# Performance work log

Measured on AMD Instinct MI355X. Metric: run time of the kernel, lower is better.

The kernel has to match this reference:

```python
import jax, jax.numpy as jnp
import numpy as np

B = 4
MAX_N = 2048
D = 512
H = 8
HD = D // H
SRC_LENS = [2048, 1536, 1800, 1200]   # sum = 6584
REF_LENS = [1900, 2048, 1400, 1600]   # sum = 6948
NEG_INF = -1e9


def setup_inputs() -> dict:
    key = jax.random.key(0)
    ks = jax.random.split(key, 8)
    n_src, n_ref = sum(SRC_LENS), sum(REF_LENS)
    s = 0.02
    return {
        "feats_src": jax.random.normal(ks[0], (n_src, D), dtype=jnp.float32),
        "batch_src": jnp.asarray(np.repeat(np.arange(B), SRC_LENS), dtype=jnp.int32),
        "feats_ref": jax.random.normal(ks[1], (n_ref, D), dtype=jnp.float32),
        "batch_ref": jnp.asarray(np.repeat(np.arange(B), REF_LENS), dtype=jnp.int32),
        "w_in": jax.random.normal(ks[2], (3 * D, D), dtype=jnp.float32) * s,
        "b_in": jnp.zeros((3 * D,), dtype=jnp.float32),
        "w_out": jax.random.normal(ks[3], (D, D), dtype=jnp.float32) * s,
        "b_out": jnp.zeros((D,), dtype=jnp.float32),
        "gw1": jax.random.normal(ks[4], (D, D), dtype=jnp.float32) * s,
        "gb1": jnp.zeros((D,), dtype=jnp.float32),
        "gw2": jax.random.normal(ks[5], (1, D), dtype=jnp.float32) * s,
        "gb2": jnp.zeros((1,), dtype=jnp.float32),
    }


def _to_dense(feats, batch_idx):
    # sparse [N, D] (sorted batch indices) -> dense [B, MAX_N, D] + key_padding_mask
    n = feats.shape[0]
    counts = jax.ops.segment_sum(jnp.ones((n,), jnp.int32), batch_idx, num_segments=B)
    starts = jnp.concatenate([jnp.zeros((1,), jnp.int32), jnp.cumsum(counts)[:-1].astype(jnp.int32)])
    pos = jnp.arange(n, dtype=jnp.int32) - starts[batch_idx]  # position within batch
    dense = jnp.zeros((B, MAX_N, feats.shape[1]), feats.dtype).at[batch_idx, pos].set(feats)
    mask = jnp.arange(MAX_N)[None, :] >= counts[:, None]  # True = padding (key_padding_mask)
    return dense, mask, pos


def reference(feats_src, batch_src, feats_ref, batch_ref,
              w_in, b_in, w_out, b_out, gw1, gb1, gw2, gb2):
    d_src, mask_src, pos_src = _to_dense(feats_src, batch_src)
    d_ref, mask_ref, _ = _to_dense(feats_ref, batch_ref)

    # nn.MultiheadAttention (batch_first, eval mode): packed in_proj, scaled dot-product
    q = (d_src @ w_in[:D].T + b_in[:D]).reshape(B, MAX_N, H, HD)
    k = (d_ref @ w_in[D:2 * D].T + b_in[D:2 * D]).reshape(B, MAX_N, H, HD)
    v = (d_ref @ w_in[2 * D:].T + b_in[2 * D:]).reshape(B, MAX_N, H, HD)
    scores = jnp.einsum('bqhd,bkhd->bhqk', q * (HD ** -0.5), k)
    scores = jnp.where(mask_ref[:, None, None, :], NEG_INF, scores)
    attn = jax.nn.softmax(scores, axis=-1)
    ctx = jnp.einsum('bhqk,bkhd->bqhd', attn, v).reshape(B, MAX_N, D)
    d_aligned = ctx @ w_out.T + b_out

    # gate MLP: Linear -> ReLU -> Linear -> Sigmoid
    gate = jax.nn.sigmoid(jax.nn.relu(d_aligned @ gw1.T + gb1) @ gw2.T + gb2)  # [B, MAX_N, 1]
    d_out = d_src + gate * d_aligned

    # dense -> ragged: gather each token back to its flat slot
    out_flat = d_out[batch_src, pos_src]  # [N_src, D]
    return out_flat, gate
```

## Files before the change

### kernel.cpp

```cpp
#include <hip/hip_runtime.h>
#include <hip/hip_bf16.h>


typedef __bf16 bf16x8_t __attribute__((ext_vector_type(8)));
typedef __bf16 bf16x4_t __attribute__((ext_vector_type(4)));
typedef float f32x4_t __attribute__((ext_vector_type(4)));
typedef float f32x2_t __attribute__((ext_vector_type(2)));

#define CQ_SCALE 0.18033688011112042f

__device__ inline bf16x8_t zero8() {
  bf16x8_t z;
#pragma unroll
  for (int t = 0; t < 8; ++t) z[t] = (__bf16)0.0f;
  return z;
}

__device__ __forceinline__ int sniff_f32(const void* w) {
  unsigned short u = ((const unsigned short*)w)[threadIdx.x & 63];
  return __ballot((u & 0x7F80) >= 0x3F80) != 0ULL;
}

__global__ void sentinel_k(float* out) {
  if (threadIdx.x == 0 && blockIdx.x == 0) out[0] = 1000.0f;
}

__global__ void cv_all(const void* w_in, const void* b_in, const void* w_out,
                       const void* b_out, const void* gw1, const void* gb1,
                       const void* gw2, const void* gb2,
                       __hip_bfloat16* __restrict__ ws) {
  int f = sniff_f32(w_in);
  const size_t F_W_IN = 16, F_B_IN = 786448, F_W_OUT = 787984, F_B_OUT = 1050128,
               F_GW1 = 1050640, F_GB1 = 1312784, F_GW2 = 1313296, F_GB2 = 1313808;
  const int total = 1313793;
  for (int g = blockIdx.x * 256 + threadIdx.x; g < total; g += gridDim.x * 256) {
    const void* src;
    size_t dst;
    int i;
    if (g < 786432) { src = w_in; dst = F_W_IN; i = g; }
    else if (g < 787968) { src = b_in; dst = F_B_IN; i = g - 786432; }
    else if (g < 1050112) { src = w_out; dst = F_W_OUT; i = g - 787968; }
    else if (g < 1050624) { src = b_out; dst = F_B_OUT; i = g - 1050112; }
    else if (g < 1312768) { src = gw1; dst = F_GW1; i = g - 1050624; }
    else if (g < 1313280) { src = gb1; dst = F_GB1; i = g - 1312768; }
    else if (g < 1313792) { src = gw2; dst = F_GW2; i = g - 1313280; }
    else { src = gb2; dst = F_GB2; i = g - 1313792; }
    ws[dst + i] = f ? __float2bfloat16(((const float*)src)[i])
                    : ((const __hip_bfloat16*)src)[i];
  }
}

__device__ __forceinline__ void gemm_core(
    const void* __restrict__ A_, long aoff, const __hip_bfloat16* __restrict__ Bt,
    const __hip_bfloat16* __restrict__ bias, __hip_bfloat16* __restrict__ C,
    int M, int K, int lda, int ldc, float cscale, int relu, int f, int bm, int bn,
    long chs, __bf16 (&As)[128][64], __bf16 (&Bs)[128][64]) {
  int tid = threadIdx.x, lane = tid & 63, wave = tid >> 6;
  int wm = wave >> 1, wn = wave & 1;
  int l15 = lane & 15, quad = lane >> 4;

  f32x4_t acc[4][4];
#pragma unroll
  for (int i = 0; i < 4; ++i)
#pragma unroll
    for (int j = 0; j < 4; ++j)
#pragma unroll
      for (int r = 0; r < 4; ++r) acc[i][j][r] = 0.f;

  bf16x8_t ra[4], rb[4];
  f32x4_t raf[4][2];

  auto gload = [&](int k0) {
#pragma unroll
    for (int s = 0; s < 4; ++s) {
      int id = s * 256 + tid;
      int row = id >> 3, col = (id & 7) * 8;
      int arow = bm + row;
      if (f) {
        if (arow < M) {
          const float* p = (const float*)A_ + aoff + (size_t)arow * lda + k0 + col;
          raf[s][0] = *reinterpret_cast<const f32x4_t*>(p);
          raf[s][1] = *reinterpret_cast<const f32x4_t*>(p + 4);
        } else {
#pragma unroll
          for (int e = 0; e < 4; ++e) { raf[s][0][e] = 0.f; raf[s][1][e] = 0.f; }
        }
      } else {
        ra[s] = (arow < M)
                    ? *reinterpret_cast<const bf16x8_t*>((const __hip_bfloat16*)A_ + aoff +
                                                         (size_t)arow * lda + k0 + col)
                    : zero8();
      }
      rb[s] = *reinterpret_cast<const bf16x8_t*>(Bt + (size_t)(bn + row) * 512 + k0 + col);
    }
  };
  auto stage = [&]() {
#pragma unroll
    for (int s = 0; s < 4; ++s) {
      int id = s * 256 + tid;
      int row = id >> 3, col = (id & 7) * 8;
      if (f) {
        bf16x8_t t;
#pragma unroll
        for (int e = 0; e < 4; ++e) {
          t[e] = (__bf16)raf[s][0][e];
          t[4 + e] = (__bf16)raf[s][1][e];
        }
        *reinterpret_cast<bf16x8_t*>(&As[row][col]) = t;
      } else {
        *reinterpret_cast<bf16x8_t*>(&As[row][col]) = ra[s];
      }
      *reinterpret_cast<bf16x8_t*>(&Bs[row][col]) = rb[s];
    }
  };

  int nk = K >> 6;
  gload(0);
  for (int it = 0; it < nk; ++it) {
    stage();
    __syncthreads();
    if (it + 1 < nk) gload((it + 1) * 64);
#pragma unroll
    for (int ks = 0; ks < 2; ++ks) {
      bf16x8_t af[4], bfv[4];
#pragma unroll
      for (int i = 0; i < 4; ++i)
        af[i] = *reinterpret_cast<const bf16x8_t*>(
            &As[wm * 64 + i * 16 + l15][ks * 32 + quad * 8]);
#pragma unroll
      for (int j = 0; j < 4; ++j)
        bfv[j] = *reinterpret_cast<const bf16x8_t*>(
            &Bs[wn * 64 + j * 16 + l15][ks * 32 + quad * 8]);
#pragma unroll
      for (int i = 0; i < 4; ++i)
#pragma unroll
        for (int j = 0; j < 4; ++j)
          acc[i][j] = __builtin_amdgcn_mfma_f32_16x16x32_bf16(af[i], bfv[j], acc[i][j], 0, 0, 0);
    }
    __syncthreads();
  }

#pragma unroll
  for (int i = 0; i < 4; ++i)
#pragma unroll
    for (int j = 0; j < 4; ++j) {
      int col = bn + wn * 64 + j * 16 + l15;
      float bv = __bfloat162float(bias[col]);
#pragma unroll
      for (int r = 0; r < 4; ++r) {
        int row = bm + wm * 64 + i * 16 + quad * 4 + r;
        if (row < M) {
          float v = (acc[i][j][r] + bv) * cscale;
          if (relu) v = fmaxf(v, 0.f);
          size_t idx = chs ? ((size_t)(col >> 6) * chs + (size_t)row * 64 + (col & 63))
                           : ((size_t)row * ldc + col);
          C[idx] = __float2bfloat16(v);
        }
      }
    }
}

__global__ __launch_bounds__(256) void proj2(
    const void* __restrict__ fs, const void* __restrict__ fr,
    const __hip_bfloat16* __restrict__ ws, __hip_bfloat16* __restrict__ Q,
    __hip_bfloat16* __restrict__ KV, const void* snf) {
  __shared__ __bf16 As[128][64];
  __shared__ __bf16 Bs[128][64];
  const size_t F_W_IN = 16, F_B_IN = 786448;
  const long CHS = (long)6948 * 64;
  int f = sniff_f32(snf);
  int bid = blockIdx.x;
  if (bid < 208) {
    int bx = bid >> 2, by = bid & 3;
    gemm_core(fs, 0, ws + F_W_IN, ws + F_B_IN, Q, 6584, 512, 512, 512, CQ_SCALE, 0, f,
              bx * 128, by * 128, 0, As, Bs);
  } else {
    int k = bid - 208;
    int bx = k >> 3, by = k & 7;
    gemm_core(fr, 0, ws + F_W_IN + 262144, ws + F_B_IN + 512, KV, 6948, 512, 512, 1024,
              1.0f, 0, f, bx * 128, by * 128, CHS, As, Bs);
  }
}

template <bool AF32>
__global__ __launch_bounds__(256) void gemm128(
    const void* __restrict__ A_, long aoff, const __hip_bfloat16* __restrict__ Bt,
    const __hip_bfloat16* __restrict__ bias, __hip_bfloat16* __restrict__ C,
    int M, int K, int lda, int ldc, float cscale, int relu, long chs,
    const void* snf) {
  __shared__ __bf16 As[128][64];
  __shared__ __bf16 Bs[128][64];
  int f = 0;
  if constexpr (AF32) f = sniff_f32(snf);
  gemm_core(A_, aoff, Bt, bias, C, M, K, lda, ldc, cscale, relu, f,
            blockIdx.x * 128, blockIdx.y * 128, chs, As, Bs);
}

template <int NS>
__global__ __launch_bounds__(256) void gemm128_pv(
    const __hip_bfloat16* __restrict__ P, const float* __restrict__ L,
    const __hip_bfloat16* __restrict__ Bt, const __hip_bfloat16* __restrict__ bias,
    __hip_bfloat16* __restrict__ C, int M) {
  const size_t PSZ = 3375104;
  __shared__ __bf16 As[128][64];
  __shared__ __bf16 Bs[128][64];
  int tid = threadIdx.x, lane = tid & 63, wave = tid >> 6;
  int wm = wave >> 1, wn = wave & 1;
  int l15 = lane & 15, quad = lane >> 4;
  int bm = blockIdx.x * 128, bn = blockIdx.y * 128;

  f32x4_t acc[4][4];
#pragma unroll
  for (int i = 0; i < 4; ++i)
#pragma unroll
    for (int j = 0; j < 4; ++j)
#pragma unroll
      for (int r = 0; r < 4; ++r) acc[i][j][r] = 0.f;

  bf16x8_t rp[NS][4], rb[4];
  float rl[4][NS];

  auto gload = [&](int k0) {
    int h = k0 >> 6;
#pragma unroll
    for (int s = 0; s < 4; ++s) {
      int id = s * 256 + tid;
      int row = id >> 3, col = (id & 7) * 8;
      int arow = bm + row;
      if (arow < M) {
        size_t off = (size_t)arow * 512 + k0 + col;
#pragma unroll
        for (int i = 0; i < NS; ++i)
          rp[i][s] = *reinterpret_cast<const bf16x8_t*>(P + i * PSZ + off);
        const float* lp = &L[((size_t)arow * 8 + h) * NS];
#pragma unroll
        for (int i = 0; i < NS; ++i) rl[s][i] = lp[i];
      } else {
#pragma unroll
        for (int i = 0; i < NS; ++i) rp[i][s] = zero8();
        rl[s][0] = 1.f;
#pragma unroll
        for (int i = 1; i < NS; ++i) rl[s][i] = 0.f;
      }
      rb[s] = *reinterpret_cast<const bf16x8_t*>(Bt + (size_t)(bn + row) * 512 + k0 + col);
    }
  };
  auto stage = [&]() {
#pragma unroll
    for (int s = 0; s < 4; ++s) {
      int id = s * 256 + tid;
      int row = id >> 3, col = (id & 7) * 8;
      float sum = 0.f;
#pragma unroll
      for (int i = 0; i < NS; ++i) sum += rl[s][i];
      float sc = 1.0f / sum;
      bf16x8_t t;
#pragma unroll
      for (int e = 0; e < 8; ++e) {
        float v = 0.f;
#pragma unroll
        for (int i = 0; i < NS; ++i) v += rl[s][i] * (float)rp[i][s][e];
        t[e] = (__bf16)(v * sc);
      }
      *reinterpret_cast<bf16x8_t*>(&As[row][col]) = t;
      *reinterpret_cast<bf16x8_t*>(&Bs[row][col]) = rb[s];
    }
  };

  gload(0);
  for (int it = 0; it < 8; ++it) {
    stage();
    __syncthreads();
    if (it + 1 < 8) gload((it + 1) * 64);
#pragma unroll
    for (int ks = 0; ks < 2; ++ks) {
      bf16x8_t af[4], bfv[4];
#pragma unroll
      for (int i = 0; i < 4; ++i)
        af[i] = *reinterpret_cast<const bf16x8_t*>(
            &As[wm * 64 + i * 16 + l15][ks * 32 + quad * 8]);
#pragma unroll
      for (int j = 0; j < 4; ++j)
        bfv[j] = *reinterpret_cast<const bf16x8_t*>(
            &Bs[wn * 64 + j * 16 + l15][ks * 32 + quad * 8]);
#pragma unroll
      for (int i = 0; i < 4; ++i)
#pragma unroll
        for (int j = 0; j < 4; ++j)
          acc[i][j] = __builtin_amdgcn_mfma_f32_16x16x32_bf16(af[i], bfv[j], acc[i][j], 0, 0, 0);
    }
    __syncthreads();
  }

#pragma unroll
  for (int i = 0; i < 4; ++i)
#pragma unroll
    for (int j = 0; j < 4; ++j) {
      int col = bn + wn * 64 + j * 16 + l15;
      float bv = __bfloat162float(bias[col]);
#pragma unroll
      for (int r = 0; r < 4; ++r) {
        int row = bm + wm * 64 + i * 16 + quad * 4 + r;
        if (row < M)
          C[(size_t)row * 512 + col] = __float2bfloat16(acc[i][j][r] + bv);
      }
    }
}

__device__ __forceinline__ void flash_core(
    const __hip_bfloat16* __restrict__ Qb, const __hip_bfloat16* __restrict__ Kb,
    const __hip_bfloat16* __restrict__ Vb, __hip_bfloat16* __restrict__ OUTb,
    float* __restrict__ LPb, int lns, int nsrc, int nref, int qt, int kt0,
    int ktNfull, int do_tail, __bf16 (&VtL)[2][64][72], __bf16 (&PL)[4][32][72]) {
  int h = blockIdx.y;
  int tid = threadIdx.x, lane = tid & 63, wave = tid >> 6;
  int l15 = lane & 15, quad = lane >> 4;
  int Mb = nsrc + 1;
  int qbase = qt * 128 + wave * 32;

  bf16x8_t qfr[2][2];
#pragma unroll
  for (int g = 0; g < 2; ++g) {
    int qrow = qbase + g * 16 + l15;
#pragma unroll
    for (int ks = 0; ks < 2; ++ks)
      qfr[g][ks] = (qrow < nsrc)
                       ? *reinterpret_cast<const bf16x8_t*>(
                             Qb + (size_t)qrow * 512 + h * 64 + ks * 32 + quad * 8)
                       : zero8();
  }

  f32x4_t O[2][4];
#pragma unroll
  for (int g = 0; g < 2; ++g)
#pragma unroll
    for (int j = 0; j < 4; ++j)
#pragma unroll
      for (int r = 0; r < 4; ++r) O[g][j][r] = 0.f;

  f32x4_t Lacc[2];
#pragma unroll
  for (int g = 0; g < 2; ++g)
#pragma unroll
    for (int r = 0; r < 4; ++r) Lacc[g][r] = 0.f;
  bf16x8_t ones;
#pragma unroll
  for (int t = 0; t < 8; ++t) ones[t] = (__bf16)1.0f;

  bf16x8_t kf[8], v0, v1;
  auto loadK = [&](int k0) {
#pragma unroll
    for (int j = 0; j < 4; ++j) {
      const __hip_bfloat16* kp = Kb + (size_t)(k0 + j * 16 + l15) * 64 + quad * 8;
      kf[j * 2] = *reinterpret_cast<const bf16x8_t*>(kp);
      kf[j * 2 + 1] = *reinterpret_cast<const bf16x8_t*>(kp + 32);
    }
  };
  auto loadV = [&](int k0) {
    const __hip_bfloat16* vp = Vb + (size_t)(k0 + lane) * 64 + wave * 16;
    v0 = *reinterpret_cast<const bf16x8_t*>(vp);
    v1 = *reinterpret_cast<const bf16x8_t*>(vp + 8);
  };

  int nit = ktNfull - kt0;
  if (nit > 0) {
    loadK(kt0 * 64);
    loadV(kt0 * 64);
  }

  for (int it = 0; it < nit; ++it) {
    int k0 = (kt0 + it) * 64;
    __bf16(*Vt)[72] = VtL[it & 1];
#pragma unroll
    for (int e = 0; e < 8; ++e) {
      Vt[wave * 16 + e][lane] = v0[e];
      Vt[wave * 16 + 8 + e][lane] = v1[e];
    }
    if (it + 1 < nit) loadV(k0 + 64);

#pragma unroll
    for (int g = 0; g < 2; ++g) {
      f32x4_t St[4];
#pragma unroll
      for (int j = 0; j < 4; ++j)
#pragma unroll
        for (int r = 0; r < 4; ++r) St[j][r] = 0.f;
#pragma unroll
      for (int j = 0; j < 4; ++j)
#pragma unroll
        for (int ks = 0; ks < 2; ++ks)
          St[j] = __builtin_amdgcn_mfma_f32_16x16x32_bf16(kf[j * 2 + ks], qfr[g][ks],
                                                          St[j], 0, 0, 0);
#pragma unroll
      for (int j = 0; j < 4; ++j) {
        bf16x4_t pk;
#pragma unroll
        for (int r = 0; r < 4; ++r) pk[r] = (__bf16)exp2f(St[j][r]);
        *reinterpret_cast<bf16x4_t*>(&PL[wave][g * 16 + l15][j * 16 + quad * 4]) = pk;
      }
    }
    if (it + 1 < nit) loadK(k0 + 64);

    __syncthreads();

    bf16x8_t pa[2][2];
#pragma unroll
    for (int g = 0; g < 2; ++g)
#pragma unroll
      for (int ks = 0; ks < 2; ++ks)
        pa[g][ks] = *reinterpret_cast<const bf16x8_t*>(
            &PL[wave][g * 16 + l15][ks * 32 + quad * 8]);
#pragma unroll
    for (int g = 0; g < 2; ++g)
#pragma unroll
      for (int ks = 0; ks < 2; ++ks)
        Lacc[g] = __builtin_amdgcn_mfma_f32_16x16x32_bf16(pa[g][ks], ones, Lacc[g], 0, 0, 0);
#pragma unroll
    for (int j = 0; j < 4; ++j)
#pragma unroll
      for (int ks = 0; ks < 2; ++ks) {
        bf16x8_t vbf =
            *reinterpret_cast<const bf16x8_t*>(&Vt[j * 16 + l15][ks * 32 + quad * 8]);
#pragma unroll
        for (int g = 0; g < 2; ++g)
          O[g][j] = __builtin_amdgcn_mfma_f32_16x16x32_bf16(pa[g][ks], vbf, O[g][j], 0, 0, 0);
      }
  }

  if (do_tail) {
    int k0 = ktNfull * 64;
    __bf16(*Vt)[72] = VtL[nit & 1];
    {
      int kr = k0 + lane;
      const __hip_bfloat16* vp = Vb + (size_t)kr * 64 + wave * 16;
      bf16x8_t t0 = (kr < nref) ? *reinterpret_cast<const bf16x8_t*>(vp) : zero8();
      bf16x8_t t1 = (kr < nref) ? *reinterpret_cast<const bf16x8_t*>(vp + 8) : zero8();
#pragma unroll
      for (int e = 0; e < 8; ++e) {
        Vt[wave * 16 + e][lane] = t0[e];
        Vt[wave * 16 + 8 + e][lane] = t1[e];
      }
    }
#pragma unroll
    for (int j = 0; j < 4; ++j) {
      int kcol = k0 + j * 16 + l15;
      const __hip_bfloat16* kp = Kb + (size_t)kcol * 64 + quad * 8;
      kf[j * 2] = (kcol < nref) ? *reinterpret_cast<const bf16x8_t*>(kp) : zero8();
      kf[j * 2 + 1] = (kcol < nref) ? *reinterpret_cast<const bf16x8_t*>(kp + 32) : zero8();
    }
#pragma unroll
    for (int g = 0; g < 2; ++g) {
      f32x4_t St[4];
#pragma unroll
      for (int j = 0; j < 4; ++j)
#pragma unroll
        for (int r = 0; r < 4; ++r) St[j][r] = 0.f;
#pragma unroll
      for (int j = 0; j < 4; ++j)
#pragma unroll
        for (int ks = 0; ks < 2; ++ks)
          St[j] = __builtin_amdgcn_mfma_f32_16x16x32_bf16(kf[j * 2 + ks], qfr[g][ks],
                                                          St[j], 0, 0, 0);
#pragma unroll
      for (int j = 0; j < 4; ++j) {
        bf16x4_t pk;
#pragma unroll
        for (int r = 0; r < 4; ++r) {
          int kl = k0 + j * 16 + quad * 4 + r;
          pk[r] = (__bf16)((kl < nref) ? exp2f(St[j][r]) : 0.f);
        }
        *reinterpret_cast<bf16x4_t*>(&PL[wave][g * 16 + l15][j * 16 + quad * 4]) = pk;
      }
    }
    __syncthreads();
    bf16x8_t pa[2][2];
#pragma unroll
    for (int g = 0; g < 2; ++g)
#pragma unroll
      for (int ks = 0; ks < 2; ++ks)
        pa[g][ks] = *reinterpret_cast<const bf16x8_t*>(
            &PL[wave][g * 16 + l15][ks * 32 + quad * 8]);
#pragma unroll
    for (int g = 0; g < 2; ++g)
#pragma unroll
      for (int ks = 0; ks < 2; ++ks)
        Lacc[g] = __builtin_amdgcn_mfma_f32_16x16x32_bf16(pa[g][ks], ones, Lacc[g], 0, 0, 0);
#pragma unroll
    for (int j = 0; j < 4; ++j)
#pragma unroll
      for (int ks = 0; ks < 2; ++ks) {
        bf16x8_t vbf =
            *reinterpret_cast<const bf16x8_t*>(&Vt[j * 16 + l15][ks * 32 + quad * 8]);
#pragma unroll
        for (int g = 0; g < 2; ++g)
          O[g][j] = __builtin_amdgcn_mfma_f32_16x16x32_bf16(pa[g][ks], vbf, O[g][j], 0, 0, 0);
      }
  }

  if (LPb && l15 == 0) {
#pragma unroll
    for (int g = 0; g < 2; ++g)
#pragma unroll
      for (int r = 0; r < 4; ++r) {
        int row = qbase + g * 16 + quad * 4 + r;
        if (row < Mb) LPb[((size_t)row * 8 + h) * lns] = Lacc[g][r];
      }
  }

#pragma unroll
  for (int g = 0; g < 2; ++g)
#pragma unroll
    for (int r = 0; r < 4; ++r) {
      int row = qbase + g * 16 + quad * 4 + r;
      if (row < Mb) {
        float inv = 1.0f / Lacc[g][r];
#pragma unroll
        for (int j = 0; j < 4; ++j)
          OUTb[(size_t)row * 512 + h * 64 + j * 16 + l15] =
              __float2bfloat16(O[g][j][r] * inv);
      }
    }
}

__global__ __launch_bounds__(256, 4) void flash_all(
    const __hip_bfloat16* __restrict__ Q, const __hip_bfloat16* __restrict__ KV,
    __hip_bfloat16* __restrict__ P, float* __restrict__ L, int nsplit) {
  const int TILE_START[4] = {0, 17, 30, 45};
  const int SRC_START[4] = {0, 2048, 3584, 5384};
  const int REF_START[4] = {0, 1900, 3948, 5348};
  const int SRC_LEN[4] = {2048, 1536, 1800, 1200};
  const int REF_LEN[4] = {1900, 2048, 1400, 1600};
  const int CS[4] = {0, 2049, 3586, 5387};
  const size_t PSZ = 3375104;
  const size_t CHS = (size_t)6948 * 64;
  __shared__ __bf16 VtL[2][64][72];
  __shared__ __bf16 PL[4][32][72];
  int bid = blockIdx.x;
  int b = (bid >= TILE_START[3]) ? 3 : (bid >= TILE_START[2]) ? 2 : (bid >= TILE_START[1]) ? 1 : 0;
  int qt = bid - TILE_START[b];
  int nref = REF_LEN[b];
  int full = nref >> 6, nkt = (nref + 63) >> 6, rem = nref & 63;
  int split = blockIdx.z;
  int kt0 = (nkt * split) / nsplit;
  int ktN, tail;
  if (split == nsplit - 1) { ktN = full; tail = rem > 0; }
  else { ktN = (nkt * (split + 1)) / nsplit; tail = 0; }
  int h = blockIdx.y;
  const __hip_bfloat16* Kb = KV + (size_t)h * CHS + (size_t)REF_START[b] * 64;
  const __hip_bfloat16* Vb = KV + (size_t)(8 + h) * CHS + (size_t)REF_START[b] * 64;
  __hip_bfloat16* OUT = P + (size_t)split * PSZ;
  float* LP = (nsplit == 1) ? nullptr : (L + split + (size_t)CS[b] * 8 * nsplit);
  flash_core(Q + (size_t)SRC_START[b] * 512, Kb, Vb, OUT + (size_t)CS[b] * 512, LP,
             nsplit, SRC_LEN[b], nref, qt, kt0, ktN, tail, VtL, PL);
}

__global__ __launch_bounds__(256, 4) void flash_one(const __hip_bfloat16* __restrict__ Qb,
                                                    const __hip_bfloat16* __restrict__ KVb,
                                                    __hip_bfloat16* __restrict__ OUTb,
                                                    int nsrc, int nref, long chs) {
  __shared__ __bf16 VtL[2][64][72];
  __shared__ __bf16 PL[4][32][72];
  int h = blockIdx.y;
  const __hip_bfloat16* Kb = KVb + (size_t)h * chs;
  const __hip_bfloat16* Vb = KVb + (size_t)(8 + h) * chs;
  flash_core(Qb, Kb, Vb, OUTb, nullptr, 1, nsrc, nref, blockIdx.x, 0, nref >> 6,
             (nref & 63) > 0, VtL, PL);
}

__global__ __launch_bounds__(256) void finalize_all(
    const void* __restrict__ src, const __hip_bfloat16* __restrict__ aligned,
    const __hip_bfloat16* __restrict__ hidden, const __hip_bfloat16* __restrict__ gw2,
    const __hip_bfloat16* __restrict__ gb2, void* __restrict__ out, const void* snf) {
  int f = sniff_f32(snf);
  int lane = threadIdx.x & 63;
  int r = blockIdx.x * 4 + (threadIdx.x >> 6);
  int b = (r >= 5387) ? 3 : (r >= 3586) ? 2 : (r >= 2049) ? 1 : 0;
  const int CS[4] = {0, 2049, 3586, 5387};
  const int NSRC[4] = {2048, 1536, 1800, 1200};
  int pos = r - CS[b];

  float zacc = 0.f;
  const __hip_bfloat16* hrow = hidden + (size_t)r * 512;
#pragma unroll
  for (int t = 0; t < 8; ++t) {
    int c = lane + (t << 6);
    zacc += __bfloat162float(hrow[c]) * __bfloat162float(gw2[c]);
  }
  for (int o = 32; o; o >>= 1) zacc += __shfl_xor(zacc, o);
  zacc += __bfloat162float(gb2[0]);
  float g = 1.f / (1.f + __expf(-zacc));

  const size_t GOFF = (size_t)6584 * 512;
  if (pos < NSRC[b]) {
    size_t ib = (size_t)(r - b) * 512;
    const __hip_bfloat16* arow = aligned + (size_t)r * 512;
#pragma unroll
    for (int t = 0; t < 8; ++t) {
      int c = lane + (t << 6);
      float sv = f ? ((const float*)src)[ib + c]
                   : __bfloat162float(((const __hip_bfloat16*)src)[ib + c]);
      float val = sv + g * __bfloat162float(arow[c]);
      if (f) ((float*)out)[ib + c] = val;
      else ((__hip_bfloat16*)out)[ib + c] = __float2bfloat16(val);
    }
    if (lane == 0) {
      size_t go = GOFF + b * 2048 + pos;
      if (f) ((float*)out)[go] = g;
      else ((__hip_bfloat16*)out)[go] = __float2bfloat16(g);
    }
  } else {
    for (int p = NSRC[b] + lane; p < 2048; p += 64) {
      size_t go = GOFF + b * 2048 + p;
      if (f) ((float*)out)[go] = g;
      else ((__hip_bfloat16*)out)[go] = __float2bfloat16(g);
    }
  }
}

__global__ __launch_bounds__(256) void finalize_b(
    const void* __restrict__ src, const __hip_bfloat16* __restrict__ alnb,
    const __hip_bfloat16* __restrict__ hidb, const __hip_bfloat16* __restrict__ gw2,
    const __hip_bfloat16* __restrict__ gb2, void* __restrict__ out,
    int b, int nsrc, int src_start, const void* snf) {
  int f = sniff_f32(snf);
  int lane = threadIdx.x & 63;
  int r = blockIdx.x * 4 + (threadIdx.x >> 6);
  if (r > nsrc) return;

  float zacc = 0.f;
  const __hip_bfloat16* hrow = hidb + (size_t)r * 512;
#pragma unroll
  for (int t = 0; t < 8; ++t) {
    int c = lane + (t << 6);
    zacc += __bfloat162float(hrow[c]) * __bfloat162float(gw2[c]);
  }
  for (int o = 32; o; o >>= 1) zacc += __shfl_xor(zacc, o);
  zacc += __bfloat162float(gb2[0]);
  float g = 1.f / (1.f + __expf(-zacc));

  const size_t GOFF = (size_t)6584 * 512;
  if (r < nsrc) {
    size_t ib = (size_t)(src_start + r) * 512;
    const __hip_bfloat16* arow = alnb + (size_t)r * 512;
#pragma unroll
    for (int t = 0; t < 8; ++t) {
      int c = lane + (t << 6);
      float sv = f ? ((const float*)src)[ib + c]
                   : __bfloat162float(((const __hip_bfloat16*)src)[ib + c]);
      float val = sv + g * __bfloat162float(arow[c]);
      if (f) ((float*)out)[ib + c] = val;
      else ((__hip_bfloat16*)out)[ib + c] = __float2bfloat16(val);
    }
    if (lane == 0) {
      size_t go = GOFF + b * 2048 + r;
      if (f) ((float*)out)[go] = g;
      else ((__hip_bfloat16*)out)[go] = __float2bfloat16(g);
    }
  } else {
    for (int p = nsrc + lane; p < 2048; p += 64) {
      size_t go = GOFF + b * 2048 + p;
      if (f) ((float*)out)[go] = g;
      else ((__hip_bfloat16*)out)[go] = __float2bfloat16(g);
    }
  }
}

extern "C" void kernel_launch(void* const* d_in, const int* in_sizes, int n_in,
                              void* d_out, int out_size, void* d_ws, size_t ws_size,
                              hipStream_t stream) {
  (void)in_sizes; (void)n_in; (void)out_size;
  const void* feats_src = d_in[0];
  const void* feats_ref = d_in[2];
  const void* w_in = d_in[4];
  const void* b_in = d_in[5];
  const void* w_out = d_in[6];
  const void* b_out = d_in[7];
  const void* gw1 = d_in[8];
  const void* gb1 = d_in[9];
  const void* gw2 = d_in[10];
  const void* gb2 = d_in[11];

  const size_t F_W_IN = 16, F_B_IN = 786448, F_W_OUT = 787984, F_B_OUT = 1050128,
               F_GW1 = 1050640, F_GB1 = 1312784, F_GW2 = 1313296, F_GB2 = 1313808,
               A0 = 1313824;
  const size_t PSZ = 3375104;
  const size_t R3E = A0 + PSZ + 7114752;
  const size_t NEED_A2 = 2 * (R3E + 2 * PSZ + 210816);
  const size_t NEED_A = 2 * (R3E + PSZ);
  const size_t NEED_B = 2 * (A0 + 4259840);

  if (ws_size < NEED_B) {
    sentinel_k<<<1, 64, 0, stream>>>((float*)d_out);
    return;
  }

  __hip_bfloat16* ws = (__hip_bfloat16*)d_ws;
  cv_all<<<dim3(1024), dim3(256), 0, stream>>>(w_in, b_in, w_out, b_out, gw1, gb1, gw2,
                                               gb2, ws);

  const int SRC_LEN[4] = {2048, 1536, 1800, 1200};
  const int REF_LEN[4] = {1900, 2048, 1400, 1600};
  const int SRC_START[4] = {0, 2048, 3584, 5384};
  const int REF_START[4] = {0, 1900, 3948, 5348};
  dim3 blk(256);

  if (ws_size >= NEED_A) {
    __hip_bfloat16* R1 = ws + A0;
    __hip_bfloat16* R2 = R1 + PSZ;
    __hip_bfloat16* R3 = R2 + 7114752;
    proj2<<<dim3(648), blk, 0, stream>>>(feats_src, feats_ref, ws, R1, R2, w_in);
    int NS = (ws_size >= NEED_A2) ? 2 : 1;
    if (NS == 2) {
      float* L = (float*)(ws + R3E + 2 * PSZ);
      flash_all<<<dim3(55, 8, 2), blk, 0, stream>>>(R1, R2, R3, L, 2);
      gemm128_pv<2><<<dim3(52, 4), blk, 0, stream>>>(R3, L, ws + F_W_OUT,
                                                     ws + F_B_OUT, R1, 6588);
    } else {
      flash_all<<<dim3(55, 8, 1), blk, 0, stream>>>(R1, R2, R3, nullptr, 1);
      gemm128<false><<<dim3(52, 4), blk, 0, stream>>>(R3, 0, ws + F_W_OUT, ws + F_B_OUT,
                                                      R1, 6588, 512, 512, 512, 1.0f, 0,
                                                      0, nullptr);
    }
    gemm128<false><<<dim3(52, 4), blk, 0, stream>>>(R1, 0, ws + F_GW1, ws + F_GB1, R3,
                                                    6588, 512, 512, 512, 1.0f, 1, 0,
                                                    nullptr);
    finalize_all<<<dim3(1647), blk, 0, stream>>>(feats_src, R1, R3, ws + F_GW2,
                                                 ws + F_GB2, d_out, w_in);
  } else {
    __hip_bfloat16* W2 = ws + A0;
    __hip_bfloat16* W1 = W2 + 2097152;
    __hip_bfloat16* W3 = W1 + 1081344;
    const long CHS_B = (long)2048 * 64;
    for (int b = 0; b < 4; ++b) {
      int nsrc = SRC_LEN[b], nref = REF_LEN[b];
      gemm128<true><<<dim3((nsrc + 127) / 128, 4), blk, 0, stream>>>(
          feats_src, (long)SRC_START[b] * 512, ws + F_W_IN, ws + F_B_IN, W1, nsrc, 512,
          512, 512, CQ_SCALE, 0, 0, w_in);
      gemm128<true><<<dim3((nref + 127) / 128, 8), blk, 0, stream>>>(
          feats_ref, (long)REF_START[b] * 512, ws + F_W_IN + 262144, ws + F_B_IN + 512,
          W2, nref, 512, 512, 1024, 1.0f, 0, CHS_B, w_in);
      flash_one<<<dim3((nsrc + 128) / 128, 8), blk, 0, stream>>>(W1, W2, W3, nsrc, nref,
                                                                 CHS_B);
      gemm128<false><<<dim3((nsrc + 128) / 128, 4), blk, 0, stream>>>(
          W3, 0, ws + F_W_OUT, ws + F_B_OUT, W1, nsrc + 1, 512, 512, 512, 1.0f, 0, 0,
          nullptr);
      gemm128<false><<<dim3((nsrc + 128) / 128, 4), blk, 0, stream>>>(
          W1, 0, ws + F_GW1, ws + F_GB1, W3, nsrc + 1, 512, 512, 512, 1.0f, 1, 0,
          nullptr);
      finalize_b<<<dim3((nsrc + 4) / 4), blk, 0, stream>>>(
          feats_src, W1, W3, ws + F_GW2, ws + F_GB2, d_out, b, nsrc, SRC_START[b], w_in);
    }
  }
}
```

Baseline: 264.8 us.

## Stage K tiles through shared memory with cooperative coalesced loads

Instead of each wave loading the full 64-row K tile directly from global memory into its own registers, all 256 threads now cooperatively load the K tile once in a coalesced pattern. They stage it into a double-buffered shared-memory array, and waves read their MFMA fragments from LDS. The barrier placement changes to one sync after staging K/V and one at the end of each iteration. Launch bounds drop from 4 to 2 blocks per SM, which allows more registers but may reduce occupancy. LDS use per block also grows.

```diff
diff --git a/kernel.cpp b/kernel.cpp
--- a/kernel.cpp
+++ b/kernel.cpp
@@ -311,7 +311,8 @@
     const __hip_bfloat16* __restrict__ Qb, const __hip_bfloat16* __restrict__ Kb,
     const __hip_bfloat16* __restrict__ Vb, __hip_bfloat16* __restrict__ OUTb,
     float* __restrict__ LPb, int lns, int nsrc, int nref, int qt, int kt0,
-    int ktNfull, int do_tail, __bf16 (&VtL)[2][64][72], __bf16 (&PL)[4][32][72]) {
+    int ktNfull, int do_tail, __bf16 (&KsL)[2][64][72], __bf16 (&VtL)[2][64][72],
+    __bf16 (&PL)[4][32][72]) {
   int h = blockIdx.y;
   int tid = threadIdx.x, lane = tid & 63, wave = tid >> 6;
   int l15 = lane & 15, quad = lane >> 4;
@@ -347,13 +348,18 @@
 #pragma unroll
   for (int t = 0; t < 8; ++t) ones[t] = (__bf16)1.0f;
 
-  bf16x8_t kf[8], v0, v1;
-  auto loadK = [&](int k0) {
-#pragma unroll
-    for (int j = 0; j < 4; ++j) {
-      const __hip_bfloat16* kp = Kb + (size_t)(k0 + j * 16 + l15) * 64 + quad * 8;
-      kf[j * 2] = *reinterpret_cast<const bf16x8_t*>(kp);
-      kf[j * 2 + 1] = *reinterpret_cast<const bf16x8_t*>(kp + 32);
+  bf16x8_t krA[2], v0, v1;
+  auto gloadK = [&](int k0) {
+    const __hip_bfloat16* base = Kb + (size_t)k0 * 64 + tid * 16;
+    krA[0] = *reinterpret_cast<const bf16x8_t*>(base);
+    krA[1] = *reinterpret_cast<const bf16x8_t*>(base + 8);
+  };
+  auto stageK = [&](int buf) {
+#pragma unroll
+    for (int p = 0; p < 2; ++p) {
+      int lin = tid * 16 + p * 8;
+      int row = lin >> 6, col = lin & 63;
+      *reinterpret_cast<bf16x8_t*>(&KsL[buf][row][col]) = krA[p];
     }
   };
   auto loadV = [&](int k0) {
@@ -364,20 +370,35 @@
 
   int nit = ktNfull - kt0;
   if (nit > 0) {
-    loadK(kt0 * 64);
+    gloadK(kt0 * 64);
     loadV(kt0 * 64);
   }
 
+  int buf = 0;
   for (int it = 0; it < nit; ++it) {
     int k0 = (kt0 + it) * 64;
-    __bf16(*Vt)[72] = VtL[it & 1];
-#pragma unroll
-    for (int e = 0; e < 8; ++e) {
-      Vt[wave * 16 + e][lane] = v0[e];
-      Vt[wave * 16 + 8 + e][lane] = v1[e];
-    }
-    if (it + 1 < nit) loadV(k0 + 64);
-
+    stageK(buf);
+    {
+      __bf16(*Vt)[72] = VtL[buf];
+#pragma unroll
+      for (int e = 0; e < 8; ++e) {
+        Vt[wave * 16 + e][lane] = v0[e];
+        Vt[wave * 16 + 8 + e][lane] = v1[e];
+      }
+    }
+    __syncthreads();
+    if (it + 1 < nit) {
+      gloadK(k0 + 64);
+      loadV(k0 + 64);
+    }
+
+    bf16x8_t kf[8];
+#pragma unroll
+    for (int j = 0; j < 4; ++j)
+#pragma unroll
+      for (int ks = 0; ks < 2; ++ks)
+        kf[j * 2 + ks] = *reinterpret_cast<const bf16x8_t*>(
+            &KsL[buf][j * 16 + l15][ks * 32 + quad * 8]);
 #pragma unroll
     for (int g = 0; g < 2; ++g) {
       f32x4_t St[4];
@@ -399,9 +420,6 @@
         *reinterpret_cast<bf16x4_t*>(&PL[wave][g * 16 + l15][j * 16 + quad * 4]) = pk;
       }
     }
-    if (it + 1 < nit) loadK(k0 + 64);
-
-    __syncthreads();
 
     bf16x8_t pa[2][2];
 #pragma unroll
@@ -419,17 +437,19 @@
     for (int j = 0; j < 4; ++j)
 #pragma unroll
       for (int ks = 0; ks < 2; ++ks) {
-        bf16x8_t vbf =
-            *reinterpret_cast<const bf16x8_t*>(&Vt[j * 16 + l15][ks * 32 + quad * 8]);
+        bf16x8_t vbf = *reinterpret_cast<const bf16x8_t*>(
+            &VtL[buf][j * 16 + l15][ks * 32 + quad * 8]);
 #pragma unroll
         for (int g = 0; g < 2; ++g)
           O[g][j] = __builtin_amdgcn_mfma_f32_16x16x32_bf16(pa[g][ks], vbf, O[g][j], 0, 0, 0);
       }
+    __syncthreads();
+    buf ^= 1;
   }
 
   if (do_tail) {
     int k0 = ktNfull * 64;
-    __bf16(*Vt)[72] = VtL[nit & 1];
+    __bf16(*Vt)[72] = VtL[buf];
     {
       int kr = k0 + lane;
       const __hip_bfloat16* vp = Vb + (size_t)kr * 64 + wave * 16;
@@ -441,6 +461,7 @@
         Vt[wave * 16 + 8 + e][lane] = t1[e];
       }
     }
+    bf16x8_t kf[8];
 #pragma unroll
     for (int j = 0; j < 4; ++j) {
       int kcol = k0 + j * 16 + l15;
@@ -522,7 +543,7 @@
     }
 }
 
-__global__ __launch_bounds__(256, 4) void flash_all(
+__global__ __launch_bounds__(256, 2) void flash_all(
     const __hip_bfloat16* __restrict__ Q, const __hip_bfloat16* __restrict__ KV,
     __hip_bfloat16* __restrict__ P, float* __restrict__ L, int nsplit) {
   const int TILE_START[4] = {0, 17, 30, 45};
@@ -533,6 +554,7 @@
   const int CS[4] = {0, 2049, 3586, 5387};
   const size_t PSZ = 3375104;
   const size_t CHS = (size_t)6948 * 64;
+  __shared__ __bf16 KsL[2][64][72];
   __shared__ __bf16 VtL[2][64][72];
   __shared__ __bf16 PL[4][32][72];
   int bid = blockIdx.x;
@@ -551,20 +573,21 @@
   __hip_bfloat16* OUT = P + (size_t)split * PSZ;
   float* LP = (nsplit == 1) ? nullptr : (L + split + (size_t)CS[b] * 8 * nsplit);
   flash_core(Q + (size_t)SRC_START[b] * 512, Kb, Vb, OUT + (size_t)CS[b] * 512, LP,
-             nsplit, SRC_LEN[b], nref, qt, kt0, ktN, tail, VtL, PL);
-}
-
-__global__ __launch_bounds__(256, 4) void flash_one(const __hip_bfloat16* __restrict__ Qb,
+             nsplit, SRC_LEN[b], nref, qt, kt0, ktN, tail, KsL, VtL, PL);
+}
+
+__global__ __launch_bounds__(256, 2) void flash_one(const __hip_bfloat16* __restrict__ Qb,
                                                     const __hip_bfloat16* __restrict__ KVb,
                                                     __hip_bfloat16* __restrict__ OUTb,
                                                     int nsrc, int nref, long chs) {
+  __shared__ __bf16 KsL[2][64][72];
   __shared__ __bf16 VtL[2][64][72];
   __shared__ __bf16 PL[4][32][72];
   int h = blockIdx.y;
   const __hip_bfloat16* Kb = KVb + (size_t)h * chs;
   const __hip_bfloat16* Vb = KVb + (size_t)(8 + h) * chs;
   flash_core(Qb, Kb, Vb, OUTb, nullptr, 1, nsrc, nref, blockIdx.x, 0, nref >> 6,
-             (nref & 63) > 0, VtL, PL);
+             (nref & 63) > 0, KsL, VtL, PL);
 }
 
 __global__ __launch_bounds__(256) void finalize_all(
```

After: 241.1 us. 8.9% less time.
